# Optimization experiments

Measured on AMD Instinct MI355X. Metric: run time of the kernel, lower is better.

Reference implementation:

```python
import jax, jax.numpy as jnp
import numpy as np

K_INTERACT = 8  # k nearest context nodes per target hyperedge


def setup_inputs() -> dict:
    key = jax.random.key(0)
    ks = jax.random.split(key, 7)
    B, C, H, W = 4, 256, 64, 64
    s = 1.0 / np.sqrt(C).astype(np.float32)
    return {
        "X_target": jax.random.normal(ks[0], (B, C, H, W), jnp.float32),
        "X_context1": jax.random.normal(ks[1], (B, C, H, W), jnp.float32),
        "X_context2": jax.random.normal(ks[2], (B, C, H, W), jnp.float32),
        # HypergraphConv params: node2edge Linear (W1,b1), edge2node Linear (W2,b2)
        "W1": jax.random.normal(ks[3], (C, C), jnp.float32) * s,
        "b1": jax.random.normal(ks[4], (C,), jnp.float32) * s,
        "W2": jax.random.normal(ks[5], (C, C), jnp.float32) * s,
        "b2": jax.random.normal(ks[6], (C,), jnp.float32) * s,
    }


def _hypergraph_one(Xt, Xc, W1, b1, W2, b2, k):
    """Per-batch hypergraph message passing, sparse form of H^T X / H X.
    Xt: [N, C] target nodes, Xc: [Nc, C] context nodes.
    Edge j = {target j} U {k nearest context nodes of target j}.
    Equivalent to dense H_i [N+Nc, N] with degree normalization.
    """
    N, C = Xt.shape
    Nc = Xc.shape[0]
    # squared Euclidean cdist (same argmins as torch.cdist), knn = smallest-k
    d2 = (jnp.sum(Xt * Xt, axis=1)[:, None]
          + jnp.sum(Xc * Xc, axis=1)[None, :]
          - 2.0 * (Xt @ Xc.T))                      # [N, Nc]
    _, knn = jax.lax.top_k(-d2, k)                   # [N, k] context indices

    # node2edge linear transform on all nodes
    Xn_t = Xt @ W1 + b1                              # [N, C]
    Xn_c = Xc @ W1 + b1                              # [Nc, C]

    # X_edge = (H^T @ Xn) / deg_e ; deg_e = k+1 (self + k distinct knn)
    gathered = Xn_c[knn]                             # [N, k, C]
    X_edge = (Xn_t + gathered.sum(axis=1)) / jnp.float32(k + 1)

    # edge2node linear transform
    X_et = X_edge @ W2 + b2                          # [N, C]

    # X_node_new = (H @ X_et) / deg_v
    # target node v belongs only to edge v -> deg_v = 1
    out_t = X_et
    # context node c sums X_et[j] over edges j that selected it
    flat = knn.reshape(-1)                           # [N*k]
    contrib = jax.ops.segment_sum(
        jnp.broadcast_to(X_et[:, None, :], (N, k, C)).reshape(N * k, C),
        flat, num_segments=Nc)                       # [Nc, C]
    counts = jax.ops.segment_sum(jnp.ones((N * k,), jnp.float32),
                                 flat, num_segments=Nc)
    out_c = contrib / jnp.clip(counts, 1.0)[:, None]  # deg_v clamp_min(1)
    return out_t, out_c


def reference(X_target, X_context1, X_context2, W1, b1, W2, b2):
    B, C, H, W = X_target.shape
    N = H * W
    to_nodes = lambda x: x.transpose(0, 2, 3, 1).reshape(B, N, C)
    Xt = to_nodes(X_target)                                       # [B, N, C]
    Xc = jnp.concatenate([to_nodes(X_context1), to_nodes(X_context2)],
                         axis=1)                                  # [B, 2N, C]
    f = lambda xt, xc: _hypergraph_one(xt, xc, W1, b1, W2, b2, K_INTERACT)
    out_t, out_c = jax.vmap(f)(Xt, Xc)
    to_img = lambda x: x.reshape(B, H, W, C).transpose(0, 3, 1, 2)
    return (to_img(out_t), to_img(out_c[:, :N]), to_img(out_c[:, N:]))
```

## Files before the change

### kernel.cpp

```cpp
#include <hip/hip_runtime.h>
#include <math.h>
#include <float.h>

#define BATCH 4
#define CH    256
#define NT    4096
#define NCTX  8192
#define KI    8

#define CSEL    10
#define DNSPLIT 8
#define CTX_PER (NCTX / DNSPLIT)
#define NTILE   (CTX_PER / 32)
#define NKEY    (DNSPLIT * CSEL)
#define RESC    12

typedef __attribute__((ext_vector_type(8)))  __bf16 bf16x8;
typedef __attribute__((ext_vector_type(16))) float  f32x16;

__device__ __forceinline__ unsigned short bf16_rne(float v) {
  unsigned u = __float_as_uint(v);
  return (unsigned short)((u + 0x7fffu + ((u >> 16) & 1u)) >> 16);
}

__global__ __launch_bounds__(256) void k_transpose2(const float* __restrict__ Xt,
                                                    const float* __restrict__ Xc1,
                                                    const float* __restrict__ Xc2,
                                                    float* __restrict__ Q,
                                                    float* __restrict__ P,
                                                    unsigned short* __restrict__ XtBh,
                                                    unsigned short* __restrict__ XtBl,
                                                    unsigned short* __restrict__ XcBh,
                                                    unsigned short* __restrict__ XcBl,
                                                    float* __restrict__ nrm) {
  __shared__ float tile[64][33];
  __shared__ float ps[8][32];
  const int which = blockIdx.z >> 2, b = blockIdx.z & 3;
  const float* src;
  float* dF; unsigned short *dH, *dL; float* nrmp = nullptr;
  if (which == 0) {
    src = Xt + (long)b * CH * NT;
    dF = Q + (long)b * NT * CH;
    dH = XtBh + (long)b * NT * CH;  dL = XtBl + (long)b * NT * CH;
  } else if (which == 1) {
    src = Xc1 + (long)b * CH * NT;
    dF = P + (long)b * NCTX * CH;
    dH = XcBh + (long)b * NCTX * CH;  dL = XcBl + (long)b * NCTX * CH;
    nrmp = nrm + (long)b * NCTX;
  } else {
    src = Xc2 + (long)b * CH * NT;
    dF = P + ((long)b * NCTX + NT) * CH;
    dH = XcBh + ((long)b * NCTX + NT) * CH;  dL = XcBl + ((long)b * NCTX + NT) * CH;
    nrmp = nrm + (long)b * NCTX + NT;
  }
  const int m0 = blockIdx.x * 32, c0 = blockIdx.y * 64;
  const int tx = threadIdx.x, ty = threadIdx.y;
  float part = 0.f;
#pragma unroll
  for (int i = ty; i < 64; i += 8) {
    float v = src[(long)(c0 + i) * NT + (m0 + tx)];
    tile[i][tx] = v;
    part = fmaf(v, v, part);
  }
  if (which) ps[ty][tx] = part;
  __syncthreads();
#pragma unroll
  for (int i = ty; i < 32; i += 8) {
    float v0 = tile[2 * tx][i];
    float v1 = tile[2 * tx + 1][i];
    long o = (long)(m0 + i) * CH + (c0 + 2 * tx);
    float2 f2; f2.x = v0; f2.y = v1;
    *(float2*)&dF[o] = f2;
    unsigned short h0 = bf16_rne(v0), h1 = bf16_rne(v1);
    ushort2 h2; h2.x = h0; h2.y = h1;
    *(ushort2*)&dH[o] = h2;
    float hf0 = __uint_as_float((unsigned)h0 << 16);
    float hf1 = __uint_as_float((unsigned)h1 << 16);
    ushort2 l2; l2.x = bf16_rne(v0 - hf0); l2.y = bf16_rne(v1 - hf1);
    *(ushort2*)&dL[o] = l2;
  }
  if (which && ty == 0) {
    float s = 0.f;
#pragma unroll
    for (int j = 0; j < 8; ++j) s += ps[j][tx];
    atomicAdd(&nrmp[m0 + tx], -0.5f * s);
  }
}

__global__ __launch_bounds__(256) void k_wtrans(const float* __restrict__ W1,
                                                const float* __restrict__ W2,
                                                unsigned short* __restrict__ WT1h,
                                                unsigned short* __restrict__ WT1l,
                                                unsigned short* __restrict__ WT2h,
                                                unsigned short* __restrict__ WT2l) {
  __shared__ float tile[32][33];
  const float* W = blockIdx.z ? W2 : W1;
  unsigned short* WTh = blockIdx.z ? WT2h : WT1h;
  unsigned short* WTl = blockIdx.z ? WT2l : WT1l;
  const int n0 = blockIdx.x * 32, k0 = blockIdx.y * 32;
  const int tx = threadIdx.x, ty = threadIdx.y;
#pragma unroll
  for (int i = ty; i < 32; i += 8)
    tile[i][tx] = W[(k0 + i) * CH + (n0 + tx)];
  __syncthreads();
#pragma unroll
  for (int i = ty; i < 32; i += 8) {
    float v = tile[tx][i];
    int o = (n0 + i) * CH + (k0 + tx);
    unsigned short h = bf16_rne(v);
    WTh[o] = h;
    float hf = __uint_as_float((unsigned)h << 16);
    WTl[o] = bf16_rne(v - hf);
  }
}

__global__ __launch_bounds__(256) void k_dist_mfma(const __bf16* __restrict__ XcB,
                                                   const __bf16* __restrict__ XtB,
                                                   const float* __restrict__ nrm,
                                                   unsigned* __restrict__ cand) {
  __shared__ __bf16 lds[2][32 * CH];
  const int lid = blockIdx.x;
  const int xk = lid & 7, rest = lid >> 3;
  const int b = xk >> 1, jh = xk & 1;
  const int jw = rest & 15, split = rest >> 4;
  const int t = threadIdx.x, w = t >> 6, lane = t & 63;
  const int l31 = lane & 31, lh = lane >> 5;
  const int tgt0 = (jh * 16 + jw) * 128 + w * 32;
  const int cbase = split * CTX_PER;
  const float* nrmt = nrm + (long)b * NCTX + cbase;

  const __bf16* tp = XtB + ((long)b * NT + tgt0 + l31) * CH + lh * 8;
  bf16x8 bfrag[16];
#pragma unroll
  for (int s = 0; s < 16; ++s) bfrag[s] = *(const bf16x8*)(tp + s * 16);

  unsigned kd[CSEL];
#pragma unroll
  for (int q = 0; q < CSEL; ++q) kd[q] = 0xFFFFFFFFu;

  const __bf16* cp = XcB + ((long)b * NCTX + cbase + l31) * CH;

  auto STAGE = [&](int buf, int jt) {
#pragma unroll
    for (int r = 0; r < 4; ++r) {
      int c = r * 4 + w;
      const __bf16* src = cp + (long)jt * 32 * CH + (c * 2 + lh) * 8;
      __bf16* dst = &lds[buf][c * 512];
      __builtin_amdgcn_global_load_lds((const __attribute__((address_space(1))) void*)src,
                                       (__attribute__((address_space(3))) void*)dst,
                                       16, 0, 0);
    }
  };

  STAGE(0, 0);
  __syncthreads();

  int cur = 0;
  for (int jt = 0; jt < NTILE; ++jt) {
    if (jt + 1 < NTILE) STAGE(cur ^ 1, jt + 1);

    const int ct0 = jt * 32;
    f32x16 acc;
#pragma unroll
    for (int g = 0; g < 4; ++g) {
      float4 nv = *(const float4*)&nrmt[ct0 + 8 * g + 4 * lh];
      acc[4 * g + 0] = nv.x; acc[4 * g + 1] = nv.y;
      acc[4 * g + 2] = nv.z; acc[4 * g + 3] = nv.w;
    }
#pragma unroll
    for (int s = 0; s < 16; ++s) {
      bf16x8 a = *(const bf16x8*)(&lds[cur][s * 512 + lane * 8]);
      acc = __builtin_amdgcn_mfma_f32_32x32x16_bf16(a, bfrag[s], acc, 0, 0, 0);
    }

#pragma unroll
    for (int reg = 0; reg < 16; ++reg) {
      const int row = (reg & 3) + 8 * (reg >> 2) + lh * 4;
      float sc = fmaf(acc[reg], -2.0f, 512.0f);
      unsigned key = (__float_as_uint(sc) & 0xFFFFF800u) | (unsigned)ct0 | (unsigned)row;
      if (__any(key < kd[CSEL - 1])) {
#pragma unroll
        for (int q = 0; q < CSEL; ++q) {
          unsigned lo = min(key, kd[q]);
          key = max(key, kd[q]);
          kd[q] = lo;
        }
      }
    }
    __syncthreads();
    cur ^= 1;
  }

  unsigned oth[CSEL];
#pragma unroll
  for (int q = 0; q < CSEL; ++q) oth[q] = (unsigned)__shfl_xor((int)kd[q], 32, 64);
  if (lh == 0) {
    long ob = (((long)b * NT + tgt0 + l31) * DNSPLIT + split) * CSEL;
#pragma unroll
    for (int q = 0; q < CSEL; ++q)
      cand[ob + q] = min(kd[q], oth[CSEL - 1 - q]);
  }
}

__global__ __launch_bounds__(64) void k_rescore(const float* __restrict__ XtT,
                                                const float* __restrict__ XcT,
                                                const unsigned* __restrict__ cand,
                                                int* __restrict__ knn,
                                                unsigned* __restrict__ counts) {
  const int n = blockIdx.x, b = blockIdx.y, lane = threadIdx.x;
  const int grp = lane >> 4, gl = lane & 15;
  __shared__ unsigned sk[NKEY];
  __shared__ int cidx[RESC];
  __shared__ double sd[RESC];
  __shared__ int sj[RESC];
  const unsigned* kp = cand + ((long)b * NT + n) * NKEY;
  unsigned k0 = kp[lane];
  unsigned k1 = (lane < NKEY - 64) ? kp[64 + lane] : 0xFFFFFFFFu;
  sk[lane] = k0;
  if (lane < NKEY - 64) sk[64 + lane] = k1;
  __syncthreads();
  int r0 = 0, r1 = 0;
  for (int i = 0; i < NKEY; ++i) {
    unsigned s = sk[i];
    r0 += (s < k0 || (s == k0 && i < lane)) ? 1 : 0;
    r1 += (s < k1 || (s == k1 && i < 64 + lane)) ? 1 : 0;
  }
  if (r0 < RESC) cidx[r0] = (lane / CSEL) * CTX_PER + (int)(k0 & 0x7FFu);
  if (lane < NKEY - 64 && r1 < RESC)
    cidx[r1] = ((64 + lane) / CSEL) * CTX_PER + (int)(k1 & 0x7FFu);
  __syncthreads();

  const float* xt = XtT + ((long)b * NT + n) * CH + gl * 16;
  double xa[16];
#pragma unroll
  for (int r = 0; r < 4; ++r) {
    float4 v = *(const float4*)(xt + r * 4);
    xa[4 * r + 0] = (double)v.x; xa[4 * r + 1] = (double)v.y;
    xa[4 * r + 2] = (double)v.z; xa[4 * r + 3] = (double)v.w;
  }
#pragma unroll
  for (int q0 = 0; q0 < RESC; q0 += 4) {
    int q = q0 + grp;
    int j = cidx[q];
    const float* xc = XcT + ((long)b * NCTX + j) * CH + gl * 16;
    double acc = 0.0;
#pragma unroll
    for (int r = 0; r < 4; ++r) {
      float4 v = *(const float4*)(xc + r * 4);
      double d0 = xa[4 * r + 0] - (double)v.x; acc = fma(d0, d0, acc);
      double d1 = xa[4 * r + 1] - (double)v.y; acc = fma(d1, d1, acc);
      double d2 = xa[4 * r + 2] - (double)v.z; acc = fma(d2, d2, acc);
      double d3 = xa[4 * r + 3] - (double)v.w; acc = fma(d3, d3, acc);
    }
#pragma unroll
    for (int off = 8; off > 0; off >>= 1) acc += __shfl_xor(acc, off, 64);
    if (gl == 0) { sd[q] = acc; sj[q] = j; }
  }
  __syncthreads();
  double dq = (lane < RESC) ? sd[lane] : DBL_MAX;
  int    jq = (lane < RESC) ? sj[lane] : 0x7fffffff;
  int rank = 0;
#pragma unroll
  for (int i = 0; i < RESC; ++i) {
    double di = sd[i]; int ji = sj[i];
    rank += (di < dq || (di == dq && ji < jq)) ? 1 : 0;
  }
  if (lane < RESC && rank < KI) {
    knn[((long)b * NT + n) * KI + rank] = jq;
    atomicAdd(&counts[(long)b * NCTX + jq], 1u);
  }
}

__global__ __launch_bounds__(256) void k_gemm_mfma(const unsigned short* __restrict__ Ah,
                                                   const unsigned short* __restrict__ Al,
                                                   const unsigned short* __restrict__ WTh,
                                                   const unsigned short* __restrict__ WTl,
                                                   const float* __restrict__ bias,
                                                   float* __restrict__ out, int M) {
  __shared__ __bf16 ldsH[32 * CH];
  __shared__ __bf16 ldsL[32 * CH];
  const int b = blockIdx.y;
  const int m0 = blockIdx.x * 32;
  const int t = threadIdx.x, w = t >> 6, lane = t & 63;
  const int l31 = lane & 31, lh = lane >> 5;
  const long abase = (long)b * M * CH;
  const unsigned short* pH = Ah + abase + (long)(m0 + l31) * CH;
  const unsigned short* pL = Al + abase + (long)(m0 + l31) * CH;
#pragma unroll
  for (int r = 0; r < 4; ++r) {
    int c = r * 4 + w;
    __builtin_amdgcn_global_load_lds(
        (const __attribute__((address_space(1))) void*)(pH + (c * 2 + lh) * 8),
        (__attribute__((address_space(3))) void*)&ldsH[c * 512], 16, 0, 0);
    __builtin_amdgcn_global_load_lds(
        (const __attribute__((address_space(1))) void*)(pL + (c * 2 + lh) * 8),
        (__attribute__((address_space(3))) void*)&ldsL[c * 512], 16, 0, 0);
  }
  __syncthreads();

  const int n0 = w * 64;
  f32x16 acc0, acc1;
#pragma unroll
  for (int i = 0; i < 16; ++i) { acc0[i] = 0.f; acc1[i] = 0.f; }
#pragma unroll
  for (int s = 0; s < 16; ++s) {
    bf16x8 ah = *(const bf16x8*)&ldsH[s * 512 + lane * 8];
    bf16x8 al = *(const bf16x8*)&ldsL[s * 512 + lane * 8];
    const int koff = lh * 8 + s * 16;
    bf16x8 bh0 = *(const bf16x8*)&WTh[(n0 + l31) * CH + koff];
    bf16x8 bl0 = *(const bf16x8*)&WTl[(n0 + l31) * CH + koff];
    bf16x8 bh1 = *(const bf16x8*)&WTh[(n0 + 32 + l31) * CH + koff];
    bf16x8 bl1 = *(const bf16x8*)&WTl[(n0 + 32 + l31) * CH + koff];
    acc0 = __builtin_amdgcn_mfma_f32_32x32x16_bf16(ah, bh0, acc0, 0, 0, 0);
    acc1 = __builtin_amdgcn_mfma_f32_32x32x16_bf16(ah, bh1, acc1, 0, 0, 0);
    acc0 = __builtin_amdgcn_mfma_f32_32x32x16_bf16(ah, bl0, acc0, 0, 0, 0);
    acc1 = __builtin_amdgcn_mfma_f32_32x32x16_bf16(ah, bl1, acc1, 0, 0, 0);
    acc0 = __builtin_amdgcn_mfma_f32_32x32x16_bf16(al, bh0, acc0, 0, 0, 0);
    acc1 = __builtin_amdgcn_mfma_f32_32x32x16_bf16(al, bh1, acc1, 0, 0, 0);
  }
  float* ob = out + abase;
  float bi0 = bias[n0 + l31], bi1 = bias[n0 + 32 + l31];
#pragma unroll
  for (int reg = 0; reg < 16; ++reg) {
    int row = (reg & 3) + 8 * (reg >> 2) + 4 * lh;
    ob[(long)(m0 + row) * CH + n0 + l31]      = acc0[reg] + bi0;
    ob[(long)(m0 + row) * CH + n0 + 32 + l31] = acc1[reg] + bi1;
  }
}

__global__ __launch_bounds__(256) void k_gg2(const float* __restrict__ Xn_c,
                                             const int* __restrict__ knn,
                                             const unsigned short* __restrict__ WTh,
                                             const unsigned short* __restrict__ WTl,
                                             const float* __restrict__ bias,
                                             float* __restrict__ out_t,
                                             float* __restrict__ R) {
  __shared__ char smem[34816];
  int* knn_s = (int*)smem;
  __bf16* XeH = (__bf16*)(smem + 1024);
  __bf16* XeL = (__bf16*)(smem + 17408);
  const int b = blockIdx.y;
  const int m0 = blockIdx.x * 32;
  const int t = threadIdx.x, w = t >> 6, lane = t & 63;
  const int l31 = lane & 31, lh = lane >> 5;

  knn_s[t] = knn[((long)b * NT + m0 + (t >> 3)) * KI + (t & 7)];
  __syncthreads();

  const int n = t & 31, cg = t >> 5;
  int idx[KI];
#pragma unroll
  for (int q = 0; q < KI; ++q) idx[q] = knn_s[n * KI + q];
  const float* trow = R + ((long)b * NT + m0 + n) * CH;
  const float* cb = Xn_c + (long)b * NCTX * CH;
#pragma unroll
  for (int kk = 0; kk < 4; ++kk) {
    const int c = cg * 32 + kk * 8;
    float xe[8];
    float4 a0 = *(const float4*)(trow + c);
    float4 a1 = *(const float4*)(trow + c + 4);
    xe[0]=a0.x; xe[1]=a0.y; xe[2]=a0.z; xe[3]=a0.w;
    xe[4]=a1.x; xe[5]=a1.y; xe[6]=a1.z; xe[7]=a1.w;
#pragma unroll
    for (int q = 0; q < KI; ++q) {
      const float* crow = cb + (long)idx[q] * CH + c;
      float4 c0 = *(const float4*)(crow);
      float4 c1 = *(const float4*)(crow + 4);
      xe[0]+=c0.x; xe[1]+=c0.y; xe[2]+=c0.z; xe[3]+=c0.w;
      xe[4]+=c1.x; xe[5]+=c1.y; xe[6]+=c1.z; xe[7]+=c1.w;
    }
    unsigned h8[8], l8[8];
#pragma unroll
    for (int e = 0; e < 8; ++e) {
      float v = xe[e] / 9.0f;
      unsigned short h = bf16_rne(v);
      h8[e] = h;
      float hf = __uint_as_float((unsigned)h << 16);
      l8[e] = bf16_rne(v - hf);
    }
    const int k8 = cg * 4 + kk;
    const int off = (k8 >> 1) * 512 + ((k8 & 1) * 32 + n) * 8;
    uint4 ph, pl;
    ph.x = h8[0] | (h8[1] << 16); ph.y = h8[2] | (h8[3] << 16);
    ph.z = h8[4] | (h8[5] << 16); ph.w = h8[6] | (h8[7] << 16);
    pl.x = l8[0] | (l8[1] << 16); pl.y = l8[2] | (l8[3] << 16);
    pl.z = l8[4] | (l8[5] << 16); pl.w = l8[6] | (l8[7] << 16);
    *(uint4*)(XeH + off) = ph;
    *(uint4*)(XeL + off) = pl;
  }
  __syncthreads();

  const unsigned short* wh0 = WTh + (long)(w * 64 + l31) * CH;
  const unsigned short* wl0 = WTl + (long)(w * 64 + l31) * CH;
  f32x16 acc0, acc1;
#pragma unroll
  for (int i = 0; i < 16; ++i) { acc0[i] = 0.f; acc1[i] = 0.f; }
#pragma unroll
  for (int s = 0; s < 16; ++s) {
    const int koff = lh * 8 + s * 16;
    bf16x8 beh = *(const bf16x8*)&XeH[s * 512 + lane * 8];
    bf16x8 bel = *(const bf16x8*)&XeL[s * 512 + lane * 8];
    bf16x8 ah0 = *(const bf16x8*)(const __bf16*)(wh0 + koff);
    bf16x8 al0 = *(const bf16x8*)(const __bf16*)(wl0 + koff);
    bf16x8 ah1 = *(const bf16x8*)(const __bf16*)(wh0 + 32 * CH + koff);
    bf16x8 al1 = *(const bf16x8*)(const __bf16*)(wl0 + 32 * CH + koff);
    acc0 = __builtin_amdgcn_mfma_f32_32x32x16_bf16(ah0, beh, acc0, 0, 0, 0);
    acc1 = __builtin_amdgcn_mfma_f32_32x32x16_bf16(ah1, beh, acc1, 0, 0, 0);
    acc0 = __builtin_amdgcn_mfma_f32_32x32x16_bf16(al0, beh, acc0, 0, 0, 0);
    acc1 = __builtin_amdgcn_mfma_f32_32x32x16_bf16(al1, beh, acc1, 0, 0, 0);
    acc0 = __builtin_amdgcn_mfma_f32_32x32x16_bf16(ah0, bel, acc0, 0, 0, 0);
    acc1 = __builtin_amdgcn_mfma_f32_32x32x16_bf16(ah1, bel, acc1, 0, 0, 0);
  }
  __syncthreads();

  float* S = (float*)smem;
  float* ot = out_t + (long)b * CH * NT + m0;
#pragma unroll
  for (int reg = 0; reg < 16; ++reg) {
    const int row = (reg & 3) + 8 * (reg >> 2) + 4 * lh;
    const int ch0 = w * 64 + row, ch1 = ch0 + 32;
    float v0 = acc0[reg] + bias[ch0];
    float v1 = acc1[reg] + bias[ch1];
    S[ch0 * 33 + l31] = v0;
    S[ch1 * 33 + l31] = v1;
    ot[(long)ch0 * NT + l31] = v0;
    ot[(long)ch1 * NT + l31] = v1;
  }
  __syncthreads();
  float* rrow = R + ((long)b * NT + m0 + n) * CH;
#pragma unroll
  for (int kk = 0; kk < 8; ++kk) {
    const int c = cg * 32 + kk * 4;
    float4 v;
    v.x = S[(c + 0) * 33 + n];
    v.y = S[(c + 1) * 33 + n];
    v.z = S[(c + 2) * 33 + n];
    v.w = S[(c + 3) * 33 + n];
    *(float4*)(rrow + c) = v;
  }
}

__global__ __launch_bounds__(256) void k_scatter(const float* __restrict__ Xet,
                                                 const int* __restrict__ knn,
                                                 float* __restrict__ contrib) {
  const int n = blockIdx.x, b = blockIdx.y, c = threadIdx.x;
  const float v = Xet[((long)b * NT + n) * CH + c];
  const int* kn = knn + ((long)b * NT + n) * KI;
#pragma unroll
  for (int q = 0; q < KI; ++q)
    atomicAdd(&contrib[((long)b * NCTX + kn[q]) * CH + c], v);
}

__global__ __launch_bounds__(256) void k_fin_c(const float* __restrict__ contrib,
                                               const unsigned* __restrict__ counts,
                                               float* __restrict__ out1,
                                               float* __restrict__ out2) {
  __shared__ float tile[32][33];
  const int b = blockIdx.z;
  const int j0 = blockIdx.x * 32, c0 = blockIdx.y * 32;
  const int tx = threadIdx.x, ty = threadIdx.y;
#pragma unroll
  for (int i = ty; i < 32; i += 8) {
    float cnt = fmaxf((float)counts[(long)b * NCTX + j0 + i], 1.0f);
    tile[i][tx] = contrib[((long)b * NCTX + j0 + i) * CH + c0 + tx] / cnt;
  }
  __syncthreads();
  float* outp = (j0 < NT) ? (out1 + (long)b * CH * NT + j0)
                          : (out2 + (long)b * CH * NT + (j0 - NT));
#pragma unroll
  for (int i = ty; i < 32; i += 8)
    outp[(long)(c0 + i) * NT + tx] = tile[tx][i];
}

extern "C" void kernel_launch(void* const* d_in, const int* in_sizes, int n_in,
                              void* d_out, int out_size, void* d_ws, size_t ws_size,
                              hipStream_t stream) {
  const float* Xt  = (const float*)d_in[0];
  const float* Xc1 = (const float*)d_in[1];
  const float* Xc2 = (const float*)d_in[2];
  const float* W1  = (const float*)d_in[3];
  const float* b1  = (const float*)d_in[4];
  const float* W2  = (const float*)d_in[5];
  const float* b2  = (const float*)d_in[6];
  float* out = (float*)d_out;

  float* P = (float*)d_ws;
  float* Q = P + (long)BATCH * NCTX * CH;
  float* R = Q + (long)BATCH * NT * CH;
  float* nrm = R + (long)BATCH * NT * CH;
  unsigned* counts = (unsigned*)(nrm + (long)BATCH * NCTX);
  int* knn = (int*)(counts + (long)BATCH * NCTX);
  unsigned short* WT1h = (unsigned short*)(knn + (long)BATCH * NT * KI);
  unsigned short* WT1l = WT1h + CH * CH;
  unsigned short* WT2h = WT1l + CH * CH;
  unsigned short* WT2l = WT2h + CH * CH;

  unsigned* cand = (unsigned*)R;

  unsigned short* XcBh = (unsigned short*)d_out;
  unsigned short* XtBh = XcBh + (long)BATCH * NCTX * CH;
  unsigned short* XcBl = XtBh + (long)BATCH * NT * CH;
  unsigned short* XtBl = XcBl + (long)BATCH * NCTX * CH;

  float* Xn_c = P;
  float* Xn_t = R;

  float* out_t  = out;
  float* out_c1 = out + (long)BATCH * CH * NT;
  float* out_c2 = out + 2L * BATCH * CH * NT;

  dim3 tb(32, 8);

  hipMemsetAsync(nrm, 0, (size_t)BATCH * NCTX * 8, stream);

  k_wtrans<<<dim3(8, 8, 2), tb, 0, stream>>>(W1, W2, WT1h, WT1l, WT2h, WT2l);

  k_transpose2<<<dim3(NT / 32, CH / 64, 12), tb, 0, stream>>>(
      Xt, Xc1, Xc2, Q, P, XtBh, XtBl, XcBh, XcBl, nrm);

  k_dist_mfma<<<dim3(1024), 256, 0, stream>>>(
      (const __bf16*)XcBh, (const __bf16*)XtBh, nrm, cand);

  k_rescore<<<dim3(NT, BATCH), 64, 0, stream>>>(Q, P, cand, knn, counts);

  k_gemm_mfma<<<dim3(NT / 32, BATCH), 256, 0, stream>>>(XtBh, XtBl, WT1h, WT1l, b1, Xn_t, NT);
  k_gemm_mfma<<<dim3(NCTX / 32, BATCH), 256, 0, stream>>>(XcBh, XcBl, WT1h, WT1l, b1, Xn_c, NCTX);

  k_gg2<<<dim3(NT / 32, BATCH), 256, 0, stream>>>(Xn_c, knn, WT2h, WT2l, b2, out_t, R);

  hipMemsetAsync(P, 0, (size_t)BATCH * NCTX * CH * 4, stream);
  k_scatter<<<dim3(NT, BATCH), 256, 0, stream>>>(R, knn, P);
  k_fin_c<<<dim3(NCTX / 32, CH / 32, BATCH), tb, 0, stream>>>(P, counts, out_c1, out_c2);
}
```

Baseline: 484.3 us.

## Replace atomic scatter with CSR inverse-index gather; split gather from edge2node GEMM

Builds a CSR inverse adjacency (prefix-scan of counts plus an atomic fill of edge lists) so each context node gathers its incoming X_et rows and writes the transposed output directly. This replaces the float atomicAdd scatter, the large memset and the separate finalize pass. The kNN gather is moved out of the GEMM kernel into its own kernel that writes hi/lo bf16 copies, and the GEMM loads them via global_load_lds. The early-exit __any check in the distance top-k insert is also removed. The cost is extra launches, extra memory traffic for the Xe buffers, and a non-deterministic summation order within each edge list.

```diff
diff --git a/kernel.cpp b/kernel.cpp
--- a/kernel.cpp
+++ b/kernel.cpp
@@ -120,9 +120,9 @@
                                                    unsigned* __restrict__ cand) {
   __shared__ __bf16 lds[2][32 * CH];
   const int lid = blockIdx.x;
-  const int xk = lid & 7, rest = lid >> 3;
+  const int xk = lid & 7;
   const int b = xk >> 1, jh = xk & 1;
-  const int jw = rest & 15, split = rest >> 4;
+  const int jw = (lid >> 3) & 15, split = lid >> 7;
   const int t = threadIdx.x, w = t >> 6, lane = t & 63;
   const int l31 = lane & 31, lh = lane >> 5;
   const int tgt0 = (jh * 16 + jw) * 128 + w * 32;
@@ -178,13 +178,11 @@
       const int row = (reg & 3) + 8 * (reg >> 2) + lh * 4;
       float sc = fmaf(acc[reg], -2.0f, 512.0f);
       unsigned key = (__float_as_uint(sc) & 0xFFFFF800u) | (unsigned)ct0 | (unsigned)row;
-      if (__any(key < kd[CSEL - 1])) {
-#pragma unroll
-        for (int q = 0; q < CSEL; ++q) {
-          unsigned lo = min(key, kd[q]);
-          key = max(key, kd[q]);
-          kd[q] = lo;
-        }
+#pragma unroll
+      for (int q = 0; q < CSEL; ++q) {
+        unsigned lo = min(key, kd[q]);
+        key = max(key, kd[q]);
+        kd[q] = lo;
       }
     }
     __syncthreads();
@@ -271,6 +269,44 @@
   }
 }
 
+__global__ __launch_bounds__(256) void k_scan(const unsigned* __restrict__ counts,
+                                              int* __restrict__ offs,
+                                              int* __restrict__ cursor) {
+  const int b = blockIdx.x, t = threadIdx.x;
+  __shared__ int ps[256];
+  const unsigned* c = counts + (long)b * NCTX;
+  int loc[32]; int s = 0;
+#pragma unroll
+  for (int i = 0; i < 32; ++i) { loc[i] = (int)c[t * 32 + i]; s += loc[i]; }
+  ps[t] = s;
+  __syncthreads();
+  for (int off = 1; off < 256; off <<= 1) {
+    int v = (t >= off) ? ps[t - off] : 0;
+    __syncthreads();
+    ps[t] += v;
+    __syncthreads();
+  }
+  int base = t ? ps[t - 1] : 0;
+  int* ob = offs + (long)b * NCTX;
+  int* cb = cursor + (long)b * NCTX;
+#pragma unroll
+  for (int i = 0; i < 32; ++i) { ob[t * 32 + i] = base; cb[t * 32 + i] = base; base += loc[i]; }
+}
+
+__global__ __launch_bounds__(256) void k_fill(const int* __restrict__ knn,
+                                              int* __restrict__ cursor,
+                                              int* __restrict__ elist) {
+  const int idx = blockIdx.x * 256 + threadIdx.x;
+  const int b = idx >> 12, n = idx & (NT - 1);
+  const int* kn = knn + (long)idx * KI;
+#pragma unroll
+  for (int q = 0; q < KI; ++q) {
+    int j = kn[q];
+    int pos = atomicAdd(&cursor[(long)b * NCTX + j], 1);
+    elist[(long)b * NT * KI + pos] = n;
+  }
+}
+
 __global__ __launch_bounds__(256) void k_gemm_mfma(const unsigned short* __restrict__ Ah,
                                                    const unsigned short* __restrict__ Al,
                                                    const unsigned short* __restrict__ WTh,
@@ -328,65 +364,53 @@
   }
 }
 
-__global__ __launch_bounds__(256) void k_gg2(const float* __restrict__ Xn_c,
-                                             const int* __restrict__ knn,
+__global__ __launch_bounds__(256) void k_gather(const float* __restrict__ Xn_t,
+                                                const float* __restrict__ Xn_c,
+                                                const int* __restrict__ knn,
+                                                unsigned short* __restrict__ XeH,
+                                                unsigned short* __restrict__ XeL) {
+  const int n = blockIdx.x, b = blockIdx.y, c = threadIdx.x;
+  const int* kn = knn + ((long)b * NT + n) * KI;
+  int j[KI];
+#pragma unroll
+  for (int q = 0; q < KI; ++q) j[q] = kn[q];
+  float acc = Xn_t[((long)b * NT + n) * CH + c];
+#pragma unroll
+  for (int q = 0; q < KI; ++q) acc += Xn_c[((long)b * NCTX + j[q]) * CH + c];
+  float xe = acc / 9.0f;
+  long o = ((long)b * NT + n) * CH + c;
+  unsigned short h = bf16_rne(xe);
+  XeH[o] = h;
+  float hf = __uint_as_float((unsigned)h << 16);
+  XeL[o] = bf16_rne(xe - hf);
+}
+
+__global__ __launch_bounds__(256) void k_g2f(const unsigned short* __restrict__ XeH_g,
+                                             const unsigned short* __restrict__ XeL_g,
                                              const unsigned short* __restrict__ WTh,
                                              const unsigned short* __restrict__ WTl,
                                              const float* __restrict__ bias,
                                              float* __restrict__ out_t,
                                              float* __restrict__ R) {
   __shared__ char smem[34816];
-  int* knn_s = (int*)smem;
-  __bf16* XeH = (__bf16*)(smem + 1024);
-  __bf16* XeL = (__bf16*)(smem + 17408);
+  __bf16* ldsH = (__bf16*)smem;
+  __bf16* ldsL = (__bf16*)(smem + 16384);
   const int b = blockIdx.y;
   const int m0 = blockIdx.x * 32;
   const int t = threadIdx.x, w = t >> 6, lane = t & 63;
   const int l31 = lane & 31, lh = lane >> 5;
-
-  knn_s[t] = knn[((long)b * NT + m0 + (t >> 3)) * KI + (t & 7)];
-  __syncthreads();
-
-  const int n = t & 31, cg = t >> 5;
-  int idx[KI];
-#pragma unroll
-  for (int q = 0; q < KI; ++q) idx[q] = knn_s[n * KI + q];
-  const float* trow = R + ((long)b * NT + m0 + n) * CH;
-  const float* cb = Xn_c + (long)b * NCTX * CH;
-#pragma unroll
-  for (int kk = 0; kk < 4; ++kk) {
-    const int c = cg * 32 + kk * 8;
-    float xe[8];
-    float4 a0 = *(const float4*)(trow + c);
-    float4 a1 = *(const float4*)(trow + c + 4);
-    xe[0]=a0.x; xe[1]=a0.y; xe[2]=a0.z; xe[3]=a0.w;
-    xe[4]=a1.x; xe[5]=a1.y; xe[6]=a1.z; xe[7]=a1.w;
-#pragma unroll
-    for (int q = 0; q < KI; ++q) {
-      const float* crow = cb + (long)idx[q] * CH + c;
-      float4 c0 = *(const float4*)(crow);
-      float4 c1 = *(const float4*)(crow + 4);
-      xe[0]+=c0.x; xe[1]+=c0.y; xe[2]+=c0.z; xe[3]+=c0.w;
-      xe[4]+=c1.x; xe[5]+=c1.y; xe[6]+=c1.z; xe[7]+=c1.w;
-    }
-    unsigned h8[8], l8[8];
-#pragma unroll
-    for (int e = 0; e < 8; ++e) {
-      float v = xe[e] / 9.0f;
-      unsigned short h = bf16_rne(v);
-      h8[e] = h;
-      float hf = __uint_as_float((unsigned)h << 16);
-      l8[e] = bf16_rne(v - hf);
-    }
-    const int k8 = cg * 4 + kk;
-    const int off = (k8 >> 1) * 512 + ((k8 & 1) * 32 + n) * 8;
-    uint4 ph, pl;
-    ph.x = h8[0] | (h8[1] << 16); ph.y = h8[2] | (h8[3] << 16);
-    ph.z = h8[4] | (h8[5] << 16); ph.w = h8[6] | (h8[7] << 16);
-    pl.x = l8[0] | (l8[1] << 16); pl.y = l8[2] | (l8[3] << 16);
-    pl.z = l8[4] | (l8[5] << 16); pl.w = l8[6] | (l8[7] << 16);
-    *(uint4*)(XeH + off) = ph;
-    *(uint4*)(XeL + off) = pl;
+  const long abase = (long)b * NT * CH;
+  const unsigned short* pH = XeH_g + abase + (long)(m0 + l31) * CH;
+  const unsigned short* pL = XeL_g + abase + (long)(m0 + l31) * CH;
+#pragma unroll
+  for (int r = 0; r < 4; ++r) {
+    int c = r * 4 + w;
+    __builtin_amdgcn_global_load_lds(
+        (const __attribute__((address_space(1))) void*)(pH + (c * 2 + lh) * 8),
+        (__attribute__((address_space(3))) void*)&ldsH[c * 512], 16, 0, 0);
+    __builtin_amdgcn_global_load_lds(
+        (const __attribute__((address_space(1))) void*)(pL + (c * 2 + lh) * 8),
+        (__attribute__((address_space(3))) void*)&ldsL[c * 512], 16, 0, 0);
   }
   __syncthreads();
 
@@ -398,8 +422,8 @@
 #pragma unroll
   for (int s = 0; s < 16; ++s) {
     const int koff = lh * 8 + s * 16;
-    bf16x8 beh = *(const bf16x8*)&XeH[s * 512 + lane * 8];
-    bf16x8 bel = *(const bf16x8*)&XeL[s * 512 + lane * 8];
+    bf16x8 beh = *(const bf16x8*)&ldsH[s * 512 + lane * 8];
+    bf16x8 bel = *(const bf16x8*)&ldsL[s * 512 + lane * 8];
     bf16x8 ah0 = *(const bf16x8*)(const __bf16*)(wh0 + koff);
     bf16x8 al0 = *(const bf16x8*)(const __bf16*)(wl0 + koff);
     bf16x8 ah1 = *(const bf16x8*)(const __bf16*)(wh0 + 32 * CH + koff);
@@ -427,6 +451,7 @@
     ot[(long)ch1 * NT + l31] = v1;
   }
   __syncthreads();
+  const int n = t & 31, cg = t >> 5;
   float* rrow = R + ((long)b * NT + m0 + n) * CH;
 #pragma unroll
   for (int kk = 0; kk < 8; ++kk) {
@@ -440,36 +465,43 @@
   }
 }
 
-__global__ __launch_bounds__(256) void k_scatter(const float* __restrict__ Xet,
-                                                 const int* __restrict__ knn,
-                                                 float* __restrict__ contrib) {
-  const int n = blockIdx.x, b = blockIdx.y, c = threadIdx.x;
-  const float v = Xet[((long)b * NT + n) * CH + c];
-  const int* kn = knn + ((long)b * NT + n) * KI;
-#pragma unroll
-  for (int q = 0; q < KI; ++q)
-    atomicAdd(&contrib[((long)b * NCTX + kn[q]) * CH + c], v);
-}
-
-__global__ __launch_bounds__(256) void k_fin_c(const float* __restrict__ contrib,
-                                               const unsigned* __restrict__ counts,
-                                               float* __restrict__ out1,
-                                               float* __restrict__ out2) {
-  __shared__ float tile[32][33];
-  const int b = blockIdx.z;
-  const int j0 = blockIdx.x * 32, c0 = blockIdx.y * 32;
-  const int tx = threadIdx.x, ty = threadIdx.y;
-#pragma unroll
-  for (int i = ty; i < 32; i += 8) {
-    float cnt = fmaxf((float)counts[(long)b * NCTX + j0 + i], 1.0f);
-    tile[i][tx] = contrib[((long)b * NCTX + j0 + i) * CH + c0 + tx] / cnt;
-  }
+__global__ __launch_bounds__(256) void k_ctxgather(const float* __restrict__ Xet,
+                                                   const int* __restrict__ offs,
+                                                   const unsigned* __restrict__ counts,
+                                                   const int* __restrict__ elist,
+                                                   float* __restrict__ out1,
+                                                   float* __restrict__ out2) {
+  __shared__ float S[32][257];
+  const int b = blockIdx.y, j0 = blockIdx.x * 32;
+  const int t = threadIdx.x;
+  const int nl = t >> 3, sub = t & 7;
+  const int j = j0 + nl;
+  const int off = offs[(long)b * NCTX + j];
+  const int deg = (int)counts[(long)b * NCTX + j];
+  const int* el = elist + (long)b * NT * KI;
+  const float* xb = Xet + (long)b * NT * CH + sub * 32;
+  float acc[32];
+#pragma unroll
+  for (int i = 0; i < 32; ++i) acc[i] = 0.f;
+  for (int e = 0; e < deg; ++e) {
+    const float* row = xb + (long)el[off + e] * CH;
+#pragma unroll
+    for (int r = 0; r < 8; ++r) {
+      float4 v = *(const float4*)(row + r * 4);
+      acc[r * 4 + 0] += v.x; acc[r * 4 + 1] += v.y;
+      acc[r * 4 + 2] += v.z; acc[r * 4 + 3] += v.w;
+    }
+  }
+  const float inv = 1.0f / fmaxf((float)deg, 1.0f);
+#pragma unroll
+  for (int i = 0; i < 32; ++i) S[nl][sub * 32 + i] = acc[i] * inv;
   __syncthreads();
   float* outp = (j0 < NT) ? (out1 + (long)b * CH * NT + j0)
                           : (out2 + (long)b * CH * NT + (j0 - NT));
-#pragma unroll
-  for (int i = ty; i < 32; i += 8)
-    outp[(long)(c0 + i) * NT + tx] = tile[tx][i];
+  const int tx = t & 31, ty = t >> 5;
+#pragma unroll
+  for (int c = ty; c < CH; c += 8)
+    outp[(long)c * NT + tx] = S[tx][c];
 }
 
 extern "C" void kernel_launch(void* const* d_in, const int* in_sizes, int n_in,
@@ -494,6 +526,9 @@
   unsigned short* WT1l = WT1h + CH * CH;
   unsigned short* WT2h = WT1l + CH * CH;
   unsigned short* WT2l = WT2h + CH * CH;
+  int* offs   = (int*)(WT2l + CH * CH);
+  int* cursor = offs + (long)BATCH * NCTX;
+  int* elist  = cursor + (long)BATCH * NCTX;
 
   unsigned* cand = (unsigned*)R;
 
@@ -504,6 +539,8 @@
 
   float* Xn_c = P;
   float* Xn_t = R;
+  unsigned short* XeH = (unsigned short*)Q;
+  unsigned short* XeL = XeH + (long)BATCH * NT * CH;
 
   float* out_t  = out;
   float* out_c1 = out + (long)BATCH * CH * NT;
@@ -518,17 +555,20 @@
   k_transpose2<<<dim3(NT / 32, CH / 64, 12), tb, 0, stream>>>(
       Xt, Xc1, Xc2, Q, P, XtBh, XtBl, XcBh, XcBl, nrm);
 
-  k_dist_mfma<<<dim3(1024), 256, 0, stream>>>(
+  k_dist_mfma<<<dim3(8 * 16 * DNSPLIT), 256, 0, stream>>>(
       (const __bf16*)XcBh, (const __bf16*)XtBh, nrm, cand);
 
   k_rescore<<<dim3(NT, BATCH), 64, 0, stream>>>(Q, P, cand, knn, counts);
+
+  k_scan<<<dim3(BATCH), 256, 0, stream>>>(counts, offs, cursor);
+  k_fill<<<dim3(BATCH * NT / 256), 256, 0, stream>>>(knn, cursor, elist);
 
   k_gemm_mfma<<<dim3(NT / 32, BATCH), 256, 0, stream>>>(XtBh, XtBl, WT1h, WT1l, b1, Xn_t, NT);
   k_gemm_mfma<<<dim3(NCTX / 32, BATCH), 256, 0, stream>>>(XcBh, XcBl, WT1h, WT1l, b1, Xn_c, NCTX);
 
-  k_gg2<<<dim3(NT / 32, BATCH), 256, 0, stream>>>(Xn_c, knn, WT2h, WT2l, b2, out_t, R);
-
-  hipMemsetAsync(P, 0, (size_t)BATCH * NCTX * CH * 4, stream);
-  k_scatter<<<dim3(NT, BATCH), 256, 0, stream>>>(R, knn, P);
-  k_fin_c<<<dim3(NCTX / 32, CH / 32, BATCH), tb, 0, stream>>>(P, counts, out_c1, out_c2);
-}
+  k_gather<<<dim3(NT, BATCH), 256, 0, stream>>>(Xn_t, Xn_c, knn, XeH, XeL);
+
+  k_g2f<<<dim3(NT / 32, BATCH), 256, 0, stream>>>(XeH, XeL, WT2h, WT2l, b2, out_t, R);
+
+  k_ctxgather<<<dim3(NCTX / 32, BATCH), 256, 0, stream>>>(R, offs, counts, elist, out_c1, out_c2);
+}
```

Result: faster. 467.5 us (-3.5%).

## Split gather from edge GEMM and remove wave-vote guard in top-k insertion

Applied to the files above, without the earlier changes.

The fused gather+GEMM kernel becomes two kernels. A per-row gather kernel sums the target row and its k context rows, then writes hi/lo bf16 splits to global memory. A GEMM kernel then loads these splits into LDS with global_load_lds before the MFMA edge2node transform. In the distance kernel, the __any early-out guard around the sorted-insert network is dropped, so every candidate goes through the min/max chain without a divergent branch. The split adds a global round-trip for the edge features and an extra launch, in exchange for a more coalesced gather.

```diff
diff --git a/kernel.cpp b/kernel.cpp
--- a/kernel.cpp
+++ b/kernel.cpp
@@ -120,9 +120,9 @@
                                                    unsigned* __restrict__ cand) {
   __shared__ __bf16 lds[2][32 * CH];
   const int lid = blockIdx.x;
-  const int xk = lid & 7, rest = lid >> 3;
+  const int xk = lid & 7;
   const int b = xk >> 1, jh = xk & 1;
-  const int jw = rest & 15, split = rest >> 4;
+  const int jw = (lid >> 3) & 15, split = lid >> 7;
   const int t = threadIdx.x, w = t >> 6, lane = t & 63;
   const int l31 = lane & 31, lh = lane >> 5;
   const int tgt0 = (jh * 16 + jw) * 128 + w * 32;
@@ -178,13 +178,11 @@
       const int row = (reg & 3) + 8 * (reg >> 2) + lh * 4;
       float sc = fmaf(acc[reg], -2.0f, 512.0f);
       unsigned key = (__float_as_uint(sc) & 0xFFFFF800u) | (unsigned)ct0 | (unsigned)row;
-      if (__any(key < kd[CSEL - 1])) {
-#pragma unroll
-        for (int q = 0; q < CSEL; ++q) {
-          unsigned lo = min(key, kd[q]);
-          key = max(key, kd[q]);
-          kd[q] = lo;
-        }
+#pragma unroll
+      for (int q = 0; q < CSEL; ++q) {
+        unsigned lo = min(key, kd[q]);
+        key = max(key, kd[q]);
+        kd[q] = lo;
       }
     }
     __syncthreads();
@@ -328,65 +326,53 @@
   }
 }
 
-__global__ __launch_bounds__(256) void k_gg2(const float* __restrict__ Xn_c,
-                                             const int* __restrict__ knn,
+__global__ __launch_bounds__(256) void k_gather(const float* __restrict__ Xn_t,
+                                                const float* __restrict__ Xn_c,
+                                                const int* __restrict__ knn,
+                                                unsigned short* __restrict__ XeH,
+                                                unsigned short* __restrict__ XeL) {
+  const int n = blockIdx.x, b = blockIdx.y, c = threadIdx.x;
+  const int* kn = knn + ((long)b * NT + n) * KI;
+  int j[KI];
+#pragma unroll
+  for (int q = 0; q < KI; ++q) j[q] = kn[q];
+  float acc = Xn_t[((long)b * NT + n) * CH + c];
+#pragma unroll
+  for (int q = 0; q < KI; ++q) acc += Xn_c[((long)b * NCTX + j[q]) * CH + c];
+  float xe = acc / 9.0f;
+  long o = ((long)b * NT + n) * CH + c;
+  unsigned short h = bf16_rne(xe);
+  XeH[o] = h;
+  float hf = __uint_as_float((unsigned)h << 16);
+  XeL[o] = bf16_rne(xe - hf);
+}
+
+__global__ __launch_bounds__(256) void k_g2f(const unsigned short* __restrict__ XeH_g,
+                                             const unsigned short* __restrict__ XeL_g,
                                              const unsigned short* __restrict__ WTh,
                                              const unsigned short* __restrict__ WTl,
                                              const float* __restrict__ bias,
                                              float* __restrict__ out_t,
                                              float* __restrict__ R) {
   __shared__ char smem[34816];
-  int* knn_s = (int*)smem;
-  __bf16* XeH = (__bf16*)(smem + 1024);
-  __bf16* XeL = (__bf16*)(smem + 17408);
+  __bf16* ldsH = (__bf16*)smem;
+  __bf16* ldsL = (__bf16*)(smem + 16384);
   const int b = blockIdx.y;
   const int m0 = blockIdx.x * 32;
   const int t = threadIdx.x, w = t >> 6, lane = t & 63;
   const int l31 = lane & 31, lh = lane >> 5;
-
-  knn_s[t] = knn[((long)b * NT + m0 + (t >> 3)) * KI + (t & 7)];
-  __syncthreads();
-
-  const int n = t & 31, cg = t >> 5;
-  int idx[KI];
-#pragma unroll
-  for (int q = 0; q < KI; ++q) idx[q] = knn_s[n * KI + q];
-  const float* trow = R + ((long)b * NT + m0 + n) * CH;
-  const float* cb = Xn_c + (long)b * NCTX * CH;
-#pragma unroll
-  for (int kk = 0; kk < 4; ++kk) {
-    const int c = cg * 32 + kk * 8;
-    float xe[8];
-    float4 a0 = *(const float4*)(trow + c);
-    float4 a1 = *(const float4*)(trow + c + 4);
-    xe[0]=a0.x; xe[1]=a0.y; xe[2]=a0.z; xe[3]=a0.w;
-    xe[4]=a1.x; xe[5]=a1.y; xe[6]=a1.z; xe[7]=a1.w;
-#pragma unroll
-    for (int q = 0; q < KI; ++q) {
-      const float* crow = cb + (long)idx[q] * CH + c;
-      float4 c0 = *(const float4*)(crow);
-      float4 c1 = *(const float4*)(crow + 4);
-      xe[0]+=c0.x; xe[1]+=c0.y; xe[2]+=c0.z; xe[3]+=c0.w;
-      xe[4]+=c1.x; xe[5]+=c1.y; xe[6]+=c1.z; xe[7]+=c1.w;
-    }
-    unsigned h8[8], l8[8];
-#pragma unroll
-    for (int e = 0; e < 8; ++e) {
-      float v = xe[e] / 9.0f;
-      unsigned short h = bf16_rne(v);
-      h8[e] = h;
-      float hf = __uint_as_float((unsigned)h << 16);
-      l8[e] = bf16_rne(v - hf);
-    }
-    const int k8 = cg * 4 + kk;
-    const int off = (k8 >> 1) * 512 + ((k8 & 1) * 32 + n) * 8;
-    uint4 ph, pl;
-    ph.x = h8[0] | (h8[1] << 16); ph.y = h8[2] | (h8[3] << 16);
-    ph.z = h8[4] | (h8[5] << 16); ph.w = h8[6] | (h8[7] << 16);
-    pl.x = l8[0] | (l8[1] << 16); pl.y = l8[2] | (l8[3] << 16);
-    pl.z = l8[4] | (l8[5] << 16); pl.w = l8[6] | (l8[7] << 16);
-    *(uint4*)(XeH + off) = ph;
-    *(uint4*)(XeL + off) = pl;
+  const long abase = (long)b * NT * CH;
+  const unsigned short* pH = XeH_g + abase + (long)(m0 + l31) * CH;
+  const unsigned short* pL = XeL_g + abase + (long)(m0 + l31) * CH;
+#pragma unroll
+  for (int r = 0; r < 4; ++r) {
+    int c = r * 4 + w;
+    __builtin_amdgcn_global_load_lds(
+        (const __attribute__((address_space(1))) void*)(pH + (c * 2 + lh) * 8),
+        (__attribute__((address_space(3))) void*)&ldsH[c * 512], 16, 0, 0);
+    __builtin_amdgcn_global_load_lds(
+        (const __attribute__((address_space(1))) void*)(pL + (c * 2 + lh) * 8),
+        (__attribute__((address_space(3))) void*)&ldsL[c * 512], 16, 0, 0);
   }
   __syncthreads();
 
@@ -398,8 +384,8 @@
 #pragma unroll
   for (int s = 0; s < 16; ++s) {
     const int koff = lh * 8 + s * 16;
-    bf16x8 beh = *(const bf16x8*)&XeH[s * 512 + lane * 8];
-    bf16x8 bel = *(const bf16x8*)&XeL[s * 512 + lane * 8];
+    bf16x8 beh = *(const bf16x8*)&ldsH[s * 512 + lane * 8];
+    bf16x8 bel = *(const bf16x8*)&ldsL[s * 512 + lane * 8];
     bf16x8 ah0 = *(const bf16x8*)(const __bf16*)(wh0 + koff);
     bf16x8 al0 = *(const bf16x8*)(const __bf16*)(wl0 + koff);
     bf16x8 ah1 = *(const bf16x8*)(const __bf16*)(wh0 + 32 * CH + koff);
@@ -427,6 +413,7 @@
     ot[(long)ch1 * NT + l31] = v1;
   }
   __syncthreads();
+  const int n = t & 31, cg = t >> 5;
   float* rrow = R + ((long)b * NT + m0 + n) * CH;
 #pragma unroll
   for (int kk = 0; kk < 8; ++kk) {
@@ -504,6 +491,8 @@
 
   float* Xn_c = P;
   float* Xn_t = R;
+  unsigned short* XeH = (unsigned short*)Q;
+  unsigned short* XeL = XeH + (long)BATCH * NT * CH;
 
   float* out_t  = out;
   float* out_c1 = out + (long)BATCH * CH * NT;
@@ -518,7 +507,7 @@
   k_transpose2<<<dim3(NT / 32, CH / 64, 12), tb, 0, stream>>>(
       Xt, Xc1, Xc2, Q, P, XtBh, XtBl, XcBh, XcBl, nrm);
 
-  k_dist_mfma<<<dim3(1024), 256, 0, stream>>>(
+  k_dist_mfma<<<dim3(8 * 16 * DNSPLIT), 256, 0, stream>>>(
       (const __bf16*)XcBh, (const __bf16*)XtBh, nrm, cand);
 
   k_rescore<<<dim3(NT, BATCH), 64, 0, stream>>>(Q, P, cand, knn, counts);
@@ -526,9 +515,12 @@
   k_gemm_mfma<<<dim3(NT / 32, BATCH), 256, 0, stream>>>(XtBh, XtBl, WT1h, WT1l, b1, Xn_t, NT);
   k_gemm_mfma<<<dim3(NCTX / 32, BATCH), 256, 0, stream>>>(XcBh, XcBl, WT1h, WT1l, b1, Xn_c, NCTX);
 
-  k_gg2<<<dim3(NT / 32, BATCH), 256, 0, stream>>>(Xn_c, knn, WT2h, WT2l, b2, out_t, R);
+  k_gather<<<dim3(NT, BATCH), 256, 0, stream>>>(Xn_t, Xn_c, knn, XeH, XeL);
 
   hipMemsetAsync(P, 0, (size_t)BATCH * NCTX * CH * 4, stream);
+
+  k_g2f<<<dim3(NT / 32, BATCH), 256, 0, stream>>>(XeH, XeL, WT2h, WT2l, b2, out_t, R);
+
   k_scatter<<<dim3(NT, BATCH), 256, 0, stream>>>(R, knn, P);
   k_fin_c<<<dim3(NCTX / 32, CH / 32, BATCH), tb, 0, stream>>>(P, counts, out_c1, out_c2);
 }
```

New measurement: 437.1 us. -9.7%, faster.
